# Optimization experiments

Measured on AMD Instinct MI355X. Metric: run time of the kernel, lower is better.

Reference implementation:

```python
import jax, jax.numpy as jnp
import numpy as np

MUL = 32      # multiplicity of each irrep type: 32x0e + 32x1o (dim = 32 + 96 = 128)
NSPEC = 10
NGRAPH = 16
EPS = 1e-5


def _split(x):
    # x: [N, 128] -> scalars [N, 32], vectors [N, 32, 3]
    return x[:, :MUL], x[:, MUL:].reshape(x.shape[0], MUL, 3)


def _cat(s, v):
    return jnp.concatenate([s, v.reshape(v.shape[0], MUL * 3)], axis=1)


def _irreps_linear(s, v, w0, w1, b0=None):
    # e3nn o3.Linear: per-irrep-type multiplicity mixing, /sqrt(fan_in), bias on scalars only
    inv = 1.0 / np.sqrt(MUL)
    s2 = s @ w0 * inv
    if b0 is not None:
        s2 = s2 + b0
    v2 = jnp.einsum('nuc,uw->nwc', v, w1) * inv
    return s2, v2


def _tensor_product(s1, v1, s2, v2, w000, w110, w011, w101):
    # SeparateWeightTensorProduct with per-path internal weights, lmax=1 paths:
    #   0e x 0e -> 0e, 1o x 1o -> 0e (CG = delta/sqrt(3)), 0e x 1o -> 1o, 1o x 0e -> 1o
    inv = 1.0 / np.sqrt(MUL * MUL)
    half = 1.0 / np.sqrt(2.0)  # two paths feed each output irrep
    out0 = (jnp.einsum('nu,nv,uvw->nw', s1, s2, w000)
            + jnp.einsum('nuc,nvc,uvw->nw', v1, v2, w110) / np.sqrt(3.0)) * (inv * half)
    out1 = (jnp.einsum('nu,nvc,uvw->nwc', s1, v2, w011)
            + jnp.einsum('nuc,nv,uvw->nwc', v1, s2, w101)) * (inv * half)
    return out0, out1


def _e3_layer_norm(s, v, batch, ln_w0, ln_b0, ln_w1):
    # per-graph equivariant layer norm: subtract mean on scalars, RMS-normalize each irrep field
    ones = jnp.ones(batch.shape, s.dtype)
    cnt = jnp.maximum(jax.ops.segment_sum(ones, batch, NGRAPH), 1.0)
    mean = jax.ops.segment_sum(s.sum(-1), batch, NGRAPH) / (cnt * MUL)
    s = s - mean[batch][:, None]
    n2s = jax.ops.segment_sum((s * s).sum(-1), batch, NGRAPH) / (cnt * MUL)
    s = s * jax.lax.rsqrt(n2s + EPS)[batch][:, None] * ln_w0 + ln_b0
    n2v = jax.ops.segment_sum((v * v).sum((-1, -2)), batch, NGRAPH) / (cnt * MUL)
    v = v * jax.lax.rsqrt(n2v + EPS)[batch][:, None, None] * ln_w1[None, :, None]
    return s, v


def setup_inputs() -> dict:
    key = jax.random.key(0)
    ks = jax.random.split(key, 24)
    N, B = 50000, 2
    rn = lambda k, sh: jax.random.normal(k, sh, dtype=jnp.float32)
    inp = {
        'node_feats_hidden': rn(ks[0], (B, N, MUL * 4)),
        'node_feats_up': rn(ks[1], (N, MUL * 4)),
        'hl_w0': rn(ks[2], (B, MUL, MUL)), 'hl_w1': rn(ks[3], (B, MUL, MUL)),
        'ul_w0': rn(ks[4], (B, MUL, MUL)), 'ul_w1': rn(ks[5], (B, MUL, MUL)),
        'tp_w000': rn(ks[6], (B, MUL, MUL, MUL)), 'tp_w110': rn(ks[7], (B, MUL, MUL, MUL)),
        'tp_w011': rn(ks[8], (B, MUL, MUL, MUL)), 'tp_w101': rn(ks[9], (B, MUL, MUL, MUL)),
        'lp_w0': rn(ks[10], (B, MUL, MUL)), 'lp_b0': jnp.zeros((B, MUL), jnp.float32),
        'lp_w1': rn(ks[11], (B, MUL, MUL)),
        'sc_w0': rn(ks[12], (B, MUL, NSPEC, MUL)), 'sc_w1': rn(ks[13], (B, MUL, NSPEC, MUL)),
        'ln_w0': jnp.ones((B, MUL), jnp.float32), 'ln_b0': jnp.zeros((B, MUL), jnp.float32),
        'ln_w1': jnp.ones((B, MUL), jnp.float32),
        'sk_w0': rn(ks[14], (B, MUL, MUL)), 'sk_b0': jnp.zeros((B, MUL), jnp.float32),
        'sk_w1': rn(ks[15], (B, MUL, MUL)),
        'node_species': jax.random.randint(ks[16], (N,), 0, NSPEC),
        'batch': jnp.sort(jax.random.randint(ks[17], (N,), 0, NGRAPH)),
    }
    return inp


def reference(node_feats_hidden, node_feats_up, hl_w0, hl_w1, ul_w0, ul_w1,
              tp_w000, tp_w110, tp_w011, tp_w101, lp_w0, lp_b0, lp_w1,
              sc_w0, sc_w1, ln_w0, ln_b0, ln_w1, sk_w0, sk_b0, sk_w1,
              node_species, batch):
    oh = jax.nn.one_hot(node_species, NSPEC, dtype=node_feats_up.dtype)
    inv_sc = 1.0 / np.sqrt(MUL * NSPEC)
    up = node_feats_up
    outs = []
    for b in range(node_feats_hidden.shape[0]):  # num_interactions blocks (fixed, small)
        sh, vh = _split(node_feats_hidden[b])
        su, vu = _split(up)
        shp, vhp = _irreps_linear(sh, vh, hl_w0[b], hl_w1[b])
        sup, vup = _irreps_linear(su, vu, ul_w0[b], ul_w1[b])
        z0, z1 = _tensor_product(shp, vhp, sup, vup,
                                 tp_w000[b], tp_w110[b], tp_w011[b], tp_w101[b])
        z0, z1 = _irreps_linear(z0, z1, lp_w0[b], lp_w1[b], lp_b0[b])
        # self connection: FullyConnectedTensorProduct(hidden, one-hot '10x0e', out)
        z0 = z0 + jnp.einsum('nu,nv,uvw->nw', sh, oh, sc_w0[b]) * inv_sc
        z1 = z1 + jnp.einsum('nuc,nv,uvw->nwc', vh, oh, sc_w1[b]) * inv_sc
        z0, z1 = _e3_layer_norm(z0, z1, batch, ln_w0[b], ln_b0[b], ln_w1[b])
        sk0, sk1 = _irreps_linear(sh, vh, sk_w0[b], sk_w1[b], sk_b0[b])
        out = _cat(z0 + sk0, z1 + sk1)
        outs.append(out)
        up = out  # next block consumes this block's output as node_feats_up
    return jnp.stack(outs)
```

## Files before the change

kernel.cpp:

```cpp
#include <hip/hip_runtime.h>
#include <math.h>

#define MULT 32
#define NSPEC 10
#define NGRAPH 16
#define NBANK 64
#define NCBANK 16
#define INV_SC 0.05590169943749474f
#define INV32S 0.17677669529663687f

typedef unsigned short u16;
typedef __bf16 v8bf __attribute__((ext_vector_type(8)));
typedef float v4f __attribute__((ext_vector_type(4)));
typedef unsigned int v4u_t __attribute__((ext_vector_type(4)));

__device__ __forceinline__ u16 f2bf(float f) {
    unsigned int u = __builtin_bit_cast(unsigned int, f);
    unsigned int r = u + 0x7fffu + ((u >> 16) & 1u);
    return (u16)(r >> 16);
}

__device__ __forceinline__ v8bf frag16(const u16* p) {
    return __builtin_bit_cast(v8bf, *(const v4u_t*)p);
}

#define MFMA(a, b, c) __builtin_amdgcn_mfma_f32_16x16x32_bf16(a, b, c, 0, 0, 0)

__global__ void zero_kernel(float* __restrict__ p, int n) {
    int i = blockIdx.x * 256 + threadIdx.x;
    if (i < n) p[i] = 0.0f;
}

__global__ void count_kernel(const int* __restrict__ batch, float* __restrict__ cntb, int N) {
    __shared__ int bins[NGRAPH];
    int t = threadIdx.x;
    if (t < NGRAPH) bins[t] = 0;
    __syncthreads();
    int i = blockIdx.x * 256 + t;
    if (i < N) atomicAdd(&bins[batch[i]], 1);
    __syncthreads();
    int bank = blockIdx.x & (NCBANK - 1);
    if (t < NGRAPH && bins[t] > 0) atomicAdd(&cntb[bank * NGRAPH + t], (float)bins[t]);
}

__global__ void stageA_kernel(const float* __restrict__ w000, const float* __restrict__ w110,
                              const float* __restrict__ w011, const float* __restrict__ w101,
                              const float* __restrict__ lp0, const float* __restrict__ lp1,
                              float* __restrict__ tmp1) {
    int gid = blockIdx.x * 256 + threadIdx.x;
    int tslot = gid >> 15;
    int e = gid & 32767;
    int z = e & 31;
    int uv = e >> 5;
    int b = tslot >> 2, path = tslot & 3;
    const float* W = (path == 0 ? w000 : path == 1 ? w110 : path == 2 ? w011 : w101) + b * 32768;
    const float* L = ((path == 0 || path == 1) ? lp0 : lp1) + b * 1024;
    float scale = (path == 1) ? (1.0f / (8192.0f * 1.7320508075688772f)) : (1.0f / 8192.0f);
    const float* wr = W + uv * 32;
    float acc = 0.0f;
    for (int w = 0; w < 32; ++w) acc += wr[w] * L[w * 32 + z];
    tmp1[gid] = acc * scale;
}

__global__ void stageB_kernel(const float* __restrict__ ul0, const float* __restrict__ ul1,
                              const float* __restrict__ tmp1, float* __restrict__ tmp2) {
    int gid = blockIdx.x * 256 + threadIdx.x;
    int tslot = gid >> 15;
    int e = gid & 32767;
    int z = e & 31;
    int bb = (e >> 5) & 31;
    int u = e >> 10;
    int b = tslot >> 2, path = tslot & 3;
    const float* U = ((path == 0 || path == 3) ? ul0 : ul1) + b * 1024;
    const float* in = tmp1 + (size_t)tslot * 32768 + u * 1024 + z;
    float acc = 0.0f;
    for (int v = 0; v < 32; ++v) acc += U[bb * 32 + v] * in[v * 32];
    tmp2[gid] = acc;
}

__global__ void stageC_kernel(const float* __restrict__ hl0, const float* __restrict__ hl1,
                              const float* __restrict__ tmp2, float* __restrict__ Weff) {
    int gid = blockIdx.x * 256 + threadIdx.x;
    int tslot = gid >> 15;
    int e = gid & 32767;
    int z = e & 31;
    int bb = (e >> 5) & 31;
    int a = e >> 10;
    int b = tslot >> 2, path = tslot & 3;
    const float* H = ((path == 0 || path == 2) ? hl0 : hl1) + b * 1024;
    const float* in = tmp2 + (size_t)tslot * 32768 + bb * 32 + z;
    float acc = 0.0f;
    for (int u = 0; u < 32; ++u) acc += H[a * 32 + u] * in[u * 1024];
    Weff[gid] = acc;
}

__global__ void pack_kernel(const float* __restrict__ Weff,
                            const float* __restrict__ sc_w0, const float* __restrict__ sc_w1,
                            u16* __restrict__ packs, int total) {
    int gid = blockIdx.x * 256 + threadIdx.x;
    if (gid >= total) return;
    int b = gid / 151552;
    int e = gid - b * 151552;
    float v;
    if (e < 131072) {
        int which = e >> 15;
        int e2 = e & 32767;
        int k = e2 & 31;
        int z = (e2 >> 5) & 31;
        int hi = e2 >> 10;
        int path = (which == 0) ? 0 : (which == 1) ? 2 : (which == 2) ? 3 : 1;
        int a  = (which < 2) ? k  : hi;
        int bb = (which < 2) ? hi : k;
        v = Weff[(size_t)((b * 4 + path) * 32 + a) * 1024 + bb * 32 + z];
    } else {
        int e2 = e - 131072;
        int which = e2 / 10240;
        int e3 = e2 - which * 10240;
        int s = e3 >> 10, z = (e3 >> 5) & 31, a = e3 & 31;
        const float* S = which ? sc_w1 : sc_w0;
        v = S[(size_t)b * 10240 + a * 320 + s * 32 + z] * INV_SC;
    }
    packs[gid] = f2bf(v);
}

__attribute__((amdgpu_waves_per_eu(4)))
__global__ __launch_bounds__(256)
void tp_kernel(const float* __restrict__ hidden_b, const float* __restrict__ up,
               const u16* __restrict__ pk,
               const float* __restrict__ lp_b0,
               const int* __restrict__ species, const int* __restrict__ batch,
               float* __restrict__ S1b, float* __restrict__ S2b, float* __restrict__ V2b,
               float* __restrict__ zout, int N) {
    constexpr int OFF_000 = 0, OFF_011 = 32768, OFF_101 = 65536, OFF_110 = 98304;
    constexpr int OFF_SC0 = 131072, OFF_SC1 = 141312;

    __shared__ __align__(16) char smem[24576];
    __shared__ int spec_l[16];
    __shared__ int bat_l[16];
    __shared__ float gs1[NGRAPH], gs2[NGRAPH], gv2[NGRAPH];

    u16* sh_bf = (u16*)smem;
    u16* su_bf = (u16*)(smem + 1280);
    u16* vu_bf = (u16*)(smem + 2560);
    u16* vh_bf = (u16*)(smem + 6400);
    float* suT = (float*)(smem + 10240);
    float* vuT = (float*)(smem + 12288);
    float* vhT = (float*)(smem + 18432);
    float* red = (float*)smem;

    const int t = threadIdx.x;
    const int w = t >> 6, lane = t & 63, quad = lane >> 4, c16 = lane & 15;
    const int n0 = blockIdx.x * 16;
    const int nvalid = min(16, N - n0);

    if (t < NGRAPH) { gs1[t] = 0.f; gs2[t] = 0.f; gv2[t] = 0.f; }
    if (t < 16) {
        spec_l[t] = (t < nvalid) ? species[n0 + t] : -1;
        bat_l[t]  = (t < nvalid) ? batch[n0 + t] : 0;
    }
    for (int i = t; i < 2048; i += 256) {
        int n = i >> 7, col = i & 127;
        float hv = 0.f, uv = 0.f;
        if (n < nvalid) {
            hv = hidden_b[(size_t)(n0 + n) * 128 + col];
            uv = up[(size_t)(n0 + n) * 128 + col];
        }
        if (col < 32) {
            sh_bf[n * 40 + col] = f2bf(hv); su_bf[n * 40 + col] = f2bf(uv);
            suT[col * 16 + n] = uv;
        } else {
            int idx = col - 32, c = idx % 3, a = idx / 3;
            vh_bf[(c * 16 + n) * 40 + a] = f2bf(hv);
            vu_bf[(c * 16 + n) * 40 + a] = f2bf(uv);
            vhT[(c * 32 + a) * 16 + n] = hv;
            vuT[(c * 32 + a) * 16 + n] = uv;
        }
    }
    __syncthreads();

    const v4f z4 = {0.f, 0.f, 0.f, 0.f};
    v4f o0[2];
    v4f o1[3][2];
    o0[0] = z4; o0[1] = z4;
#pragma unroll
    for (int c = 0; c < 3; ++c) { o1[c][0] = z4; o1[c][1] = z4; }

    v8bf a_sh = frag16(sh_bf + c16 * 40 + quad * 8);

    {
        const u16* Wb = pk + OFF_000 + (w * 16 * 16 + c16) * 32 + quad * 8;
#pragma unroll 4
        for (int th = 0; th < 8; ++th) {
            int bb = w * 8 + th;
            v4f y = *(const v4f*)(suT + bb * 16 + quad * 4);
            v8bf bf0 = frag16(Wb + (th * 2) * 512);
            v8bf bf1 = frag16(Wb + (th * 2 + 1) * 512);
            v4f C0 = MFMA(a_sh, bf0, z4);
            v4f C1 = MFMA(a_sh, bf1, z4);
#pragma unroll
            for (int r = 0; r < 4; ++r) {
                o0[0][r] += C0[r] * y[r];
                o0[1][r] += C1[r] * y[r];
            }
        }
    }
    {
        const u16* Wb = pk + OFF_011 + (w * 16 * 16 + c16) * 32 + quad * 8;
#pragma unroll 2
        for (int th = 0; th < 8; ++th) {
            int bb = w * 8 + th;
            v8bf bf0 = frag16(Wb + (th * 2) * 512);
            v8bf bf1 = frag16(Wb + (th * 2 + 1) * 512);
            v4f C0 = MFMA(a_sh, bf0, z4);
            v4f C1 = MFMA(a_sh, bf1, z4);
#pragma unroll
            for (int c = 0; c < 3; ++c) {
                v4f y = *(const v4f*)(vuT + (c * 32 + bb) * 16 + quad * 4);
#pragma unroll
                for (int r = 0; r < 4; ++r) {
                    o1[c][0][r] += C0[r] * y[r];
                    o1[c][1][r] += C1[r] * y[r];
                }
            }
        }
    }
    {
        v8bf a_su = frag16(su_bf + c16 * 40 + quad * 8);
        const u16* Wb = pk + OFF_101 + (w * 16 * 16 + c16) * 32 + quad * 8;
#pragma unroll 2
        for (int th = 0; th < 8; ++th) {
            int aa = w * 8 + th;
            v8bf bf0 = frag16(Wb + (th * 2) * 512);
            v8bf bf1 = frag16(Wb + (th * 2 + 1) * 512);
            v4f C0 = MFMA(a_su, bf0, z4);
            v4f C1 = MFMA(a_su, bf1, z4);
#pragma unroll
            for (int c = 0; c < 3; ++c) {
                v4f y = *(const v4f*)(vhT + (c * 32 + aa) * 16 + quad * 4);
#pragma unroll
                for (int r = 0; r < 4; ++r) {
                    o1[c][0][r] += C0[r] * y[r];
                    o1[c][1][r] += C1[r] * y[r];
                }
            }
        }
    }
    {
        v8bf av0 = frag16(vu_bf + (0 * 16 + c16) * 40 + quad * 8);
        v8bf av1 = frag16(vu_bf + (1 * 16 + c16) * 40 + quad * 8);
        v8bf av2 = frag16(vu_bf + (2 * 16 + c16) * 40 + quad * 8);
        const u16* Wb = pk + OFF_110 + (w * 16 * 16 + c16) * 32 + quad * 8;
#pragma unroll 2
        for (int th = 0; th < 8; ++th) {
            int aa = w * 8 + th;
            v8bf bf0 = frag16(Wb + (th * 2) * 512);
            v8bf bf1 = frag16(Wb + (th * 2 + 1) * 512);
            v4f y0 = *(const v4f*)(vhT + (0 * 32 + aa) * 16 + quad * 4);
            v4f y1 = *(const v4f*)(vhT + (1 * 32 + aa) * 16 + quad * 4);
            v4f y2 = *(const v4f*)(vhT + (2 * 32 + aa) * 16 + quad * 4);
            v4f C00 = MFMA(av0, bf0, z4), C01 = MFMA(av0, bf1, z4);
            v4f C10 = MFMA(av1, bf0, z4), C11 = MFMA(av1, bf1, z4);
            v4f C20 = MFMA(av2, bf0, z4), C21 = MFMA(av2, bf1, z4);
#pragma unroll
            for (int r = 0; r < 4; ++r) {
                o0[0][r] += C00[r] * y0[r] + C10[r] * y1[r] + C20[r] * y2[r];
                o0[1][r] += C01[r] * y0[r] + C11[r] * y1[r] + C21[r] * y2[r];
            }
        }
    }
    {
        const int s0 = (w < 2) ? w * 3 : 6 + (w - 2) * 2;
        const int ns = (w < 2) ? 3 : 2;
        v8bf zf = __builtin_bit_cast(v8bf, (v4u_t){0u, 0u, 0u, 0u});
        int sp = spec_l[c16];
        v8bf a_vh0 = frag16(vh_bf + (0 * 16 + c16) * 40 + quad * 8);
        v8bf a_vh1 = frag16(vh_bf + (1 * 16 + c16) * 40 + quad * 8);
        v8bf a_vh2 = frag16(vh_bf + (2 * 16 + c16) * 40 + quad * 8);
        for (int si = s0; si < s0 + ns; ++si) {
            bool m = (sp == si);
            v8bf ash_m = m ? a_sh : zf;
            v8bf am0 = m ? a_vh0 : zf;
            v8bf am1 = m ? a_vh1 : zf;
            v8bf am2 = m ? a_vh2 : zf;
#pragma unroll
            for (int zh = 0; zh < 2; ++zh) {
                int boff = (si * 32 + zh * 16 + c16) * 32 + quad * 8;
                v8bf bf0 = frag16(pk + OFF_SC0 + boff);
                v8bf bf1 = frag16(pk + OFF_SC1 + boff);
                o0[zh] = MFMA(ash_m, bf0, o0[zh]);
                o1[0][zh] = MFMA(am0, bf1, o1[0][zh]);
                o1[1][zh] = MFMA(am1, bf1, o1[1][zh]);
                o1[2][zh] = MFMA(am2, bf1, o1[2][zh]);
            }
        }
    }

    __syncthreads();
    if (w < 2) {
#pragma unroll
        for (int r = 0; r < 4; ++r) {
            int n = quad * 4 + r;
            float* row = red + (w * 16 + n) * 132;
            row[c16]      = o0[0][r];
            row[16 + c16] = o0[1][r];
#pragma unroll
            for (int c = 0; c < 3; ++c) {
                row[32 + c16 * 3 + c]        = o1[c][0][r];
                row[32 + (16 + c16) * 3 + c] = o1[c][1][r];
            }
        }
    }
    __syncthreads();
    if (w >= 2) {
#pragma unroll
        for (int r = 0; r < 4; ++r) {
            int n = quad * 4 + r;
            float* row = red + ((w - 2) * 16 + n) * 132;
            row[c16]      += o0[0][r];
            row[16 + c16] += o0[1][r];
#pragma unroll
            for (int c = 0; c < 3; ++c) {
                row[32 + c16 * 3 + c]        += o1[c][0][r];
                row[32 + (16 + c16) * 3 + c] += o1[c][1][r];
            }
        }
    }
    __syncthreads();
    {
        int n = t >> 4, seg = t & 15;
        v4f sa = z4, sb = z4;
#pragma unroll
        for (int ww = 0; ww < 2; ++ww) {
            const float* rp = red + (ww * 16 + n) * 132 + seg * 8;
            sa += *(const v4f*)rp;
            sb += *(const v4f*)(rp + 4);
        }
        float s1p = 0.f, s2p = 0.f, v2p = 0.f;
        if (seg < 4) {
            sa += *(const v4f*)(lp_b0 + seg * 8);
            sb += *(const v4f*)(lp_b0 + seg * 8 + 4);
            s1p = sa[0] + sa[1] + sa[2] + sa[3] + sb[0] + sb[1] + sb[2] + sb[3];
            s2p = sa[0]*sa[0] + sa[1]*sa[1] + sa[2]*sa[2] + sa[3]*sa[3]
                + sb[0]*sb[0] + sb[1]*sb[1] + sb[2]*sb[2] + sb[3]*sb[3];
        } else {
            v2p = sa[0]*sa[0] + sa[1]*sa[1] + sa[2]*sa[2] + sa[3]*sa[3]
                + sb[0]*sb[0] + sb[1]*sb[1] + sb[2]*sb[2] + sb[3]*sb[3];
        }
        if (n < nvalid) {
            float* op = zout + (size_t)(n0 + n) * 128 + seg * 8;
            *(v4f*)op = sa;
            *(v4f*)(op + 4) = sb;
        }
#pragma unroll
        for (int off = 8; off >= 1; off >>= 1) {
            s1p += __shfl_xor(s1p, off, 16);
            s2p += __shfl_xor(s2p, off, 16);
            v2p += __shfl_xor(v2p, off, 16);
        }
        if (seg == 0 && n < nvalid) {
            int g = bat_l[n];
            atomicAdd(&gs1[g], s1p);
            atomicAdd(&gs2[g], s2p);
            atomicAdd(&gv2[g], v2p);
        }
    }
    __syncthreads();
    {
        const int bank = blockIdx.x & (NBANK - 1);
        if (t < NGRAPH) {
            if (gs1[t] != 0.f) atomicAdd(&S1b[bank * NGRAPH + t], gs1[t]);
            if (gs2[t] != 0.f) atomicAdd(&S2b[bank * NGRAPH + t], gs2[t]);
            if (gv2[t] != 0.f) atomicAdd(&V2b[bank * NGRAPH + t], gv2[t]);
        }
    }
}

__global__ __launch_bounds__(256)
void norm_kernel(const float* __restrict__ hidden_b, float* __restrict__ out_b,
                 const float* __restrict__ skw0, const float* __restrict__ skb0,
                 const float* __restrict__ skw1,
                 const float* __restrict__ lnw0, const float* __restrict__ lnb0,
                 const float* __restrict__ lnw1,
                 const int* __restrict__ batch,
                 const float* __restrict__ S1b, const float* __restrict__ S2b,
                 const float* __restrict__ V2b, const float* __restrict__ cntb, int N) {
    __shared__ __align__(16) float sh_l[8][32];
    __shared__ __align__(16) float vh_l[8][96];
    __shared__ float stat_s[3][NGRAPH];
    __shared__ float cnt_s[NGRAPH];
    const int t = threadIdx.x, z = t & 31, nl = t >> 5;
    const int n0 = blockIdx.x * 8;
    for (int i = t; i < 8 * 128; i += 256) {
        int n = i >> 7, col = i & 127;
        float v = (n0 + n < N) ? hidden_b[(size_t)(n0 + n) * 128 + col] : 0.f;
        if (col < 32) sh_l[n][col] = v; else vh_l[n][col - 32] = v;
    }
    if (t < 48) {
        int arr = t >> 4, g = t & 15;
        const float* base = (arr == 0) ? S1b : (arr == 1) ? S2b : V2b;
        float s = 0.f;
        for (int k = 0; k < NBANK; ++k) s += base[k * NGRAPH + g];
        stat_s[arr][g] = s;
    } else if (t < 64) {
        int g = t - 48;
        float c = 0.f;
        for (int k = 0; k < NCBANK; ++k) c += cntb[k * NGRAPH + g];
        cnt_s[g] = c;
    }
    __syncthreads();
    const int n = n0 + nl;
    if (n >= N) return;

    float sk0 = 0.f, s1 = 0.f, s2 = 0.f, s3 = 0.f;
    for (int a = 0; a < 32; ++a) {
        float w0 = skw0[a * 32 + z];
        float w1 = skw1[a * 32 + z];
        sk0 += sh_l[nl][a] * w0;
        s1 += vh_l[nl][a * 3 + 0] * w1;
        s2 += vh_l[nl][a * 3 + 1] * w1;
        s3 += vh_l[nl][a * 3 + 2] * w1;
    }
    int g = batch[n];
    float cM = fmaxf(cnt_s[g], 1.0f) * 32.0f;
    float mean = stat_s[0][g] / cM;
    float var = fmaxf(stat_s[1][g] / cM - mean * mean, 0.0f);
    float rs = rsqrtf(var + 1e-5f);
    float rv = rsqrtf(fmaxf(stat_s[2][g] / cM, 0.0f) + 1e-5f);

    size_t base = (size_t)n * 128;
    float z0 = out_b[base + z];
    out_b[base + z] = (z0 - mean) * rs * lnw0[z] + lnb0[z] + sk0 * INV32S + skb0[z];
    float lw = lnw1[z] * rv;
    float x0 = out_b[base + 32 + z * 3 + 0];
    float x1 = out_b[base + 32 + z * 3 + 1];
    float x2 = out_b[base + 32 + z * 3 + 2];
    out_b[base + 32 + z * 3 + 0] = x0 * lw + s1 * INV32S;
    out_b[base + 32 + z * 3 + 1] = x1 * lw + s2 * INV32S;
    out_b[base + 32 + z * 3 + 2] = x2 * lw + s3 * INV32S;
}

extern "C" void kernel_launch(void* const* d_in, const int* in_sizes, int n_in,
                              void* d_out, int out_size, void* d_ws, size_t ws_size,
                              hipStream_t stream) {
    const float* hidden = (const float*)d_in[0];
    const float* up0    = (const float*)d_in[1];
    const float* hl_w0  = (const float*)d_in[2];
    const float* hl_w1  = (const float*)d_in[3];
    const float* ul_w0  = (const float*)d_in[4];
    const float* ul_w1  = (const float*)d_in[5];
    const float* w000   = (const float*)d_in[6];
    const float* w110   = (const float*)d_in[7];
    const float* w011   = (const float*)d_in[8];
    const float* w101   = (const float*)d_in[9];
    const float* lp_w0  = (const float*)d_in[10];
    const float* lp_b0  = (const float*)d_in[11];
    const float* lp_w1  = (const float*)d_in[12];
    const float* sc_w0  = (const float*)d_in[13];
    const float* sc_w1  = (const float*)d_in[14];
    const float* ln_w0  = (const float*)d_in[15];
    const float* ln_b0  = (const float*)d_in[16];
    const float* ln_w1  = (const float*)d_in[17];
    const float* sk_w0  = (const float*)d_in[18];
    const float* sk_b0  = (const float*)d_in[19];
    const float* sk_w1  = (const float*)d_in[20];
    const int* species  = (const int*)d_in[21];
    const int* batch    = (const int*)d_in[22];
    float* out = (float*)d_out;

    const int N = in_sizes[21];
    const int B = in_sizes[0] / (N * 128);

    float* ws = (float*)d_ws;
    float* tmp1 = ws;
    float* tmp2 = tmp1 + (size_t)B * 4 * 32768;
    float* cntb = tmp2 + (size_t)B * 4 * 32768;
    float* S1b = cntb + NCBANK * NGRAPH;
    float* S2b = S1b + (size_t)B * NBANK * NGRAPH;
    float* V2b = S2b + (size_t)B * NBANK * NGRAPH;
    int statn = NCBANK * NGRAPH + 3 * B * NBANK * NGRAPH;

    zero_kernel<<<(statn + 255) / 256, 256, 0, stream>>>(cntb, statn);
    count_kernel<<<(N + 255) / 256, 256, 0, stream>>>(batch, cntb, N);

    int nb = B * 4 * 32768 / 256;
    stageA_kernel<<<nb, 256, 0, stream>>>(w000, w110, w011, w101, lp_w0, lp_w1, tmp1);
    stageB_kernel<<<nb, 256, 0, stream>>>(ul_w0, ul_w1, tmp1, tmp2);
    stageC_kernel<<<nb, 256, 0, stream>>>(hl_w0, hl_w1, tmp2, tmp1);

    u16* packs = (u16*)tmp2;
    int ptotal = B * 151552;
    pack_kernel<<<(ptotal + 255) / 256, 256, 0, stream>>>(tmp1, sc_w0, sc_w1, packs, ptotal);

    for (int b = 0; b < B; ++b) {
        const float* up = (b == 0) ? up0 : out + (size_t)(b - 1) * N * 128;
        const u16* pb = packs + (size_t)b * 151552;
        tp_kernel<<<(N + 15) / 16, 256, 0, stream>>>(
            hidden + (size_t)b * N * 128, up, pb,
            lp_b0 + b * MULT, species, batch,
            S1b + (size_t)b * NBANK * NGRAPH, S2b + (size_t)b * NBANK * NGRAPH,
            V2b + (size_t)b * NBANK * NGRAPH,
            out + (size_t)b * N * 128, N);
        norm_kernel<<<(N + 7) / 8, 256, 0, stream>>>(
            hidden + (size_t)b * N * 128, out + (size_t)b * N * 128,
            sk_w0 + b * 1024, sk_b0 + b * MULT, sk_w1 + b * 1024,
            ln_w0 + b * MULT, ln_b0 + b * MULT, ln_w1 + b * MULT,
            batch, S1b + (size_t)b * NBANK * NGRAPH, S2b + (size_t)b * NBANK * NGRAPH,
            V2b + (size_t)b * NBANK * NGRAPH, cntb, N);
    }
}
```

Measured before the change: 385.2 us.

## Process two 16-node tiles per block to reuse weight fragments

```diff
diff --git a/kernel.cpp b/kernel.cpp
--- a/kernel.cpp
+++ b/kernel.cpp
@@ -123,7 +123,7 @@
     packs[gid] = f2bf(v);
 }
 
-__attribute__((amdgpu_waves_per_eu(4)))
+__attribute__((amdgpu_waves_per_eu(3)))
 __global__ __launch_bounds__(256)
 void tp_kernel(const float* __restrict__ hidden_b, const float* __restrict__ up,
                const u16* __restrict__ pk,
@@ -134,137 +134,164 @@
     constexpr int OFF_000 = 0, OFF_011 = 32768, OFF_101 = 65536, OFF_110 = 98304;
     constexpr int OFF_SC0 = 131072, OFF_SC1 = 141312;
 
-    __shared__ __align__(16) char smem[24576];
-    __shared__ int spec_l[16];
-    __shared__ int bat_l[16];
+    __shared__ __align__(16) char smem[49152];
+    __shared__ int spec_l[32];
+    __shared__ int bat_l[32];
     __shared__ float gs1[NGRAPH], gs2[NGRAPH], gv2[NGRAPH];
 
     u16* sh_bf = (u16*)smem;
-    u16* su_bf = (u16*)(smem + 1280);
-    u16* vu_bf = (u16*)(smem + 2560);
-    u16* vh_bf = (u16*)(smem + 6400);
-    float* suT = (float*)(smem + 10240);
-    float* vuT = (float*)(smem + 12288);
-    float* vhT = (float*)(smem + 18432);
+    u16* su_bf = (u16*)(smem + 2560);
+    u16* vu_bf = (u16*)(smem + 5120);
+    u16* vh_bf = (u16*)(smem + 12800);
+    float* suT = (float*)(smem + 20480);
+    float* vuT = (float*)(smem + 24576);
+    float* vhT = (float*)(smem + 36864);
     float* red = (float*)smem;
 
     const int t = threadIdx.x;
     const int w = t >> 6, lane = t & 63, quad = lane >> 4, c16 = lane & 15;
-    const int n0 = blockIdx.x * 16;
-    const int nvalid = min(16, N - n0);
+    const int n0 = blockIdx.x * 32;
+    const int nvalid = min(32, N - n0);
 
     if (t < NGRAPH) { gs1[t] = 0.f; gs2[t] = 0.f; gv2[t] = 0.f; }
-    if (t < 16) {
+    if (t < 32) {
         spec_l[t] = (t < nvalid) ? species[n0 + t] : -1;
         bat_l[t]  = (t < nvalid) ? batch[n0 + t] : 0;
     }
-    for (int i = t; i < 2048; i += 256) {
+    for (int i = t; i < 4096; i += 256) {
         int n = i >> 7, col = i & 127;
+        int tile = n >> 4, nl = n & 15;
         float hv = 0.f, uv = 0.f;
         if (n < nvalid) {
             hv = hidden_b[(size_t)(n0 + n) * 128 + col];
             uv = up[(size_t)(n0 + n) * 128 + col];
         }
         if (col < 32) {
-            sh_bf[n * 40 + col] = f2bf(hv); su_bf[n * 40 + col] = f2bf(uv);
-            suT[col * 16 + n] = uv;
+            sh_bf[tile * 640 + nl * 40 + col] = f2bf(hv);
+            su_bf[tile * 640 + nl * 40 + col] = f2bf(uv);
+            suT[tile * 512 + col * 16 + nl] = uv;
         } else {
             int idx = col - 32, c = idx % 3, a = idx / 3;
-            vh_bf[(c * 16 + n) * 40 + a] = f2bf(hv);
-            vu_bf[(c * 16 + n) * 40 + a] = f2bf(uv);
-            vhT[(c * 32 + a) * 16 + n] = hv;
-            vuT[(c * 32 + a) * 16 + n] = uv;
+            vh_bf[tile * 1920 + (c * 16 + nl) * 40 + a] = f2bf(hv);
+            vu_bf[tile * 1920 + (c * 16 + nl) * 40 + a] = f2bf(uv);
+            vhT[tile * 1536 + (c * 32 + a) * 16 + nl] = hv;
+            vuT[tile * 1536 + (c * 32 + a) * 16 + nl] = uv;
         }
     }
     __syncthreads();
 
     const v4f z4 = {0.f, 0.f, 0.f, 0.f};
-    v4f o0[2];
-    v4f o1[3][2];
-    o0[0] = z4; o0[1] = z4;
-#pragma unroll
-    for (int c = 0; c < 3; ++c) { o1[c][0] = z4; o1[c][1] = z4; }
-
-    v8bf a_sh = frag16(sh_bf + c16 * 40 + quad * 8);
-
-    {
-        const u16* Wb = pk + OFF_000 + (w * 16 * 16 + c16) * 32 + quad * 8;
+    v4f o0A[2], o1A[3][2], o0B[2], o1B[3][2];
+    o0A[0] = z4; o0A[1] = z4; o0B[0] = z4; o0B[1] = z4;
+#pragma unroll
+    for (int c = 0; c < 3; ++c) {
+        o1A[c][0] = z4; o1A[c][1] = z4;
+        o1B[c][0] = z4; o1B[c][1] = z4;
+    }
+
+    v8bf a_shA = frag16(sh_bf + c16 * 40 + quad * 8);
+    v8bf a_shB = frag16(sh_bf + 640 + c16 * 40 + quad * 8);
+
+    {
+        const u16* Wb = pk + OFF_000 + (w * 256 + c16) * 32 + quad * 8;
 #pragma unroll 4
         for (int th = 0; th < 8; ++th) {
             int bb = w * 8 + th;
-            v4f y = *(const v4f*)(suT + bb * 16 + quad * 4);
             v8bf bf0 = frag16(Wb + (th * 2) * 512);
             v8bf bf1 = frag16(Wb + (th * 2 + 1) * 512);
-            v4f C0 = MFMA(a_sh, bf0, z4);
-            v4f C1 = MFMA(a_sh, bf1, z4);
+            v4f yA = *(const v4f*)(suT + bb * 16 + quad * 4);
+            v4f yB = *(const v4f*)(suT + 512 + bb * 16 + quad * 4);
+            v4f C0 = MFMA(a_shA, bf0, z4), C1 = MFMA(a_shA, bf1, z4);
+            v4f D0 = MFMA(a_shB, bf0, z4), D1 = MFMA(a_shB, bf1, z4);
 #pragma unroll
             for (int r = 0; r < 4; ++r) {
-                o0[0][r] += C0[r] * y[r];
-                o0[1][r] += C1[r] * y[r];
-            }
-        }
-    }
-    {
-        const u16* Wb = pk + OFF_011 + (w * 16 * 16 + c16) * 32 + quad * 8;
+                o0A[0][r] += C0[r] * yA[r]; o0A[1][r] += C1[r] * yA[r];
+                o0B[0][r] += D0[r] * yB[r]; o0B[1][r] += D1[r] * yB[r];
+            }
+        }
+    }
+    {
+        const u16* Wb = pk + OFF_011 + (w * 256 + c16) * 32 + quad * 8;
 #pragma unroll 2
         for (int th = 0; th < 8; ++th) {
             int bb = w * 8 + th;
             v8bf bf0 = frag16(Wb + (th * 2) * 512);
             v8bf bf1 = frag16(Wb + (th * 2 + 1) * 512);
-            v4f C0 = MFMA(a_sh, bf0, z4);
-            v4f C1 = MFMA(a_sh, bf1, z4);
+            v4f C0 = MFMA(a_shA, bf0, z4), C1 = MFMA(a_shA, bf1, z4);
+            v4f D0 = MFMA(a_shB, bf0, z4), D1 = MFMA(a_shB, bf1, z4);
 #pragma unroll
             for (int c = 0; c < 3; ++c) {
-                v4f y = *(const v4f*)(vuT + (c * 32 + bb) * 16 + quad * 4);
+                v4f yA = *(const v4f*)(vuT + (c * 32 + bb) * 16 + quad * 4);
+                v4f yB = *(const v4f*)(vuT + 1536 + (c * 32 + bb) * 16 + quad * 4);
 #pragma unroll
                 for (int r = 0; r < 4; ++r) {
-                    o1[c][0][r] += C0[r] * y[r];
-                    o1[c][1][r] += C1[r] * y[r];
+                    o1A[c][0][r] += C0[r] * yA[r]; o1A[c][1][r] += C1[r] * yA[r];
+                    o1B[c][0][r] += D0[r] * yB[r]; o1B[c][1][r] += D1[r] * yB[r];
                 }
             }
         }
     }
     {
-        v8bf a_su = frag16(su_bf + c16 * 40 + quad * 8);
-        const u16* Wb = pk + OFF_101 + (w * 16 * 16 + c16) * 32 + quad * 8;
+        v8bf a_suA = frag16(su_bf + c16 * 40 + quad * 8);
+        v8bf a_suB = frag16(su_bf + 640 + c16 * 40 + quad * 8);
+        const u16* Wb = pk + OFF_101 + (w * 256 + c16) * 32 + quad * 8;
 #pragma unroll 2
         for (int th = 0; th < 8; ++th) {
             int aa = w * 8 + th;
             v8bf bf0 = frag16(Wb + (th * 2) * 512);
             v8bf bf1 = frag16(Wb + (th * 2 + 1) * 512);
-            v4f C0 = MFMA(a_su, bf0, z4);
-            v4f C1 = MFMA(a_su, bf1, z4);
+            v4f C0 = MFMA(a_suA, bf0, z4), C1 = MFMA(a_suA, bf1, z4);
+            v4f D0 = MFMA(a_suB, bf0, z4), D1 = MFMA(a_suB, bf1, z4);
 #pragma unroll
             for (int c = 0; c < 3; ++c) {
-                v4f y = *(const v4f*)(vhT + (c * 32 + aa) * 16 + quad * 4);
+                v4f yA = *(const v4f*)(vhT + (c * 32 + aa) * 16 + quad * 4);
+                v4f yB = *(const v4f*)(vhT + 1536 + (c * 32 + aa) * 16 + quad * 4);
 #pragma unroll
                 for (int r = 0; r < 4; ++r) {
-                    o1[c][0][r] += C0[r] * y[r];
-                    o1[c][1][r] += C1[r] * y[r];
+                    o1A[c][0][r] += C0[r] * yA[r]; o1A[c][1][r] += C1[r] * yA[r];
+                    o1B[c][0][r] += D0[r] * yB[r]; o1B[c][1][r] += D1[r] * yB[r];
                 }
             }
         }
     }
     {
-        v8bf av0 = frag16(vu_bf + (0 * 16 + c16) * 40 + quad * 8);
-        v8bf av1 = frag16(vu_bf + (1 * 16 + c16) * 40 + quad * 8);
-        v8bf av2 = frag16(vu_bf + (2 * 16 + c16) * 40 + quad * 8);
-        const u16* Wb = pk + OFF_110 + (w * 16 * 16 + c16) * 32 + quad * 8;
+        v8bf avA0 = frag16(vu_bf + (0 * 16 + c16) * 40 + quad * 8);
+        v8bf avA1 = frag16(vu_bf + (1 * 16 + c16) * 40 + quad * 8);
+        v8bf avA2 = frag16(vu_bf + (2 * 16 + c16) * 40 + quad * 8);
+        v8bf avB0 = frag16(vu_bf + 1920 + (0 * 16 + c16) * 40 + quad * 8);
+        v8bf avB1 = frag16(vu_bf + 1920 + (1 * 16 + c16) * 40 + quad * 8);
+        v8bf avB2 = frag16(vu_bf + 1920 + (2 * 16 + c16) * 40 + quad * 8);
+        const u16* Wb = pk + OFF_110 + (w * 256 + c16) * 32 + quad * 8;
 #pragma unroll 2
         for (int th = 0; th < 8; ++th) {
             int aa = w * 8 + th;
             v8bf bf0 = frag16(Wb + (th * 2) * 512);
             v8bf bf1 = frag16(Wb + (th * 2 + 1) * 512);
-            v4f y0 = *(const v4f*)(vhT + (0 * 32 + aa) * 16 + quad * 4);
-            v4f y1 = *(const v4f*)(vhT + (1 * 32 + aa) * 16 + quad * 4);
-            v4f y2 = *(const v4f*)(vhT + (2 * 32 + aa) * 16 + quad * 4);
-            v4f C00 = MFMA(av0, bf0, z4), C01 = MFMA(av0, bf1, z4);
-            v4f C10 = MFMA(av1, bf0, z4), C11 = MFMA(av1, bf1, z4);
-            v4f C20 = MFMA(av2, bf0, z4), C21 = MFMA(av2, bf1, z4);
-#pragma unroll
-            for (int r = 0; r < 4; ++r) {
-                o0[0][r] += C00[r] * y0[r] + C10[r] * y1[r] + C20[r] * y2[r];
-                o0[1][r] += C01[r] * y0[r] + C11[r] * y1[r] + C21[r] * y2[r];
+            {
+                v4f y0 = *(const v4f*)(vhT + (0 * 32 + aa) * 16 + quad * 4);
+                v4f y1 = *(const v4f*)(vhT + (1 * 32 + aa) * 16 + quad * 4);
+                v4f y2 = *(const v4f*)(vhT + (2 * 32 + aa) * 16 + quad * 4);
+                v4f C00 = MFMA(avA0, bf0, z4), C01 = MFMA(avA0, bf1, z4);
+                v4f C10 = MFMA(avA1, bf0, z4), C11 = MFMA(avA1, bf1, z4);
+                v4f C20 = MFMA(avA2, bf0, z4), C21 = MFMA(avA2, bf1, z4);
+#pragma unroll
+                for (int r = 0; r < 4; ++r) {
+                    o0A[0][r] += C00[r] * y0[r] + C10[r] * y1[r] + C20[r] * y2[r];
+                    o0A[1][r] += C01[r] * y0[r] + C11[r] * y1[r] + C21[r] * y2[r];
+                }
+            }
+            {
+                v4f y0 = *(const v4f*)(vhT + 1536 + (0 * 32 + aa) * 16 + quad * 4);
+                v4f y1 = *(const v4f*)(vhT + 1536 + (1 * 32 + aa) * 16 + quad * 4);
+                v4f y2 = *(const v4f*)(vhT + 1536 + (2 * 32 + aa) * 16 + quad * 4);
+                v4f C00 = MFMA(avB0, bf0, z4), C01 = MFMA(avB0, bf1, z4);
+                v4f C10 = MFMA(avB1, bf0, z4), C11 = MFMA(avB1, bf1, z4);
+                v4f C20 = MFMA(avB2, bf0, z4), C21 = MFMA(avB2, bf1, z4);
+#pragma unroll
+                for (int r = 0; r < 4; ++r) {
+                    o0B[0][r] += C00[r] * y0[r] + C10[r] * y1[r] + C20[r] * y2[r];
+                    o0B[1][r] += C01[r] * y0[r] + C11[r] * y1[r] + C21[r] * y2[r];
+                }
             }
         }
     }
@@ -272,25 +299,37 @@
         const int s0 = (w < 2) ? w * 3 : 6 + (w - 2) * 2;
         const int ns = (w < 2) ? 3 : 2;
         v8bf zf = __builtin_bit_cast(v8bf, (v4u_t){0u, 0u, 0u, 0u});
-        int sp = spec_l[c16];
-        v8bf a_vh0 = frag16(vh_bf + (0 * 16 + c16) * 40 + quad * 8);
-        v8bf a_vh1 = frag16(vh_bf + (1 * 16 + c16) * 40 + quad * 8);
-        v8bf a_vh2 = frag16(vh_bf + (2 * 16 + c16) * 40 + quad * 8);
+        int spA = spec_l[c16];
+        int spB = spec_l[16 + c16];
+        v8bf a_vhA0 = frag16(vh_bf + (0 * 16 + c16) * 40 + quad * 8);
+        v8bf a_vhA1 = frag16(vh_bf + (1 * 16 + c16) * 40 + quad * 8);
+        v8bf a_vhA2 = frag16(vh_bf + (2 * 16 + c16) * 40 + quad * 8);
+        v8bf a_vhB0 = frag16(vh_bf + 1920 + (0 * 16 + c16) * 40 + quad * 8);
+        v8bf a_vhB1 = frag16(vh_bf + 1920 + (1 * 16 + c16) * 40 + quad * 8);
+        v8bf a_vhB2 = frag16(vh_bf + 1920 + (2 * 16 + c16) * 40 + quad * 8);
         for (int si = s0; si < s0 + ns; ++si) {
-            bool m = (sp == si);
-            v8bf ash_m = m ? a_sh : zf;
-            v8bf am0 = m ? a_vh0 : zf;
-            v8bf am1 = m ? a_vh1 : zf;
-            v8bf am2 = m ? a_vh2 : zf;
+            bool mA = (spA == si), mB = (spB == si);
+            v8bf ashA_m = mA ? a_shA : zf;
+            v8bf amA0 = mA ? a_vhA0 : zf;
+            v8bf amA1 = mA ? a_vhA1 : zf;
+            v8bf amA2 = mA ? a_vhA2 : zf;
+            v8bf ashB_m = mB ? a_shB : zf;
+            v8bf amB0 = mB ? a_vhB0 : zf;
+            v8bf amB1 = mB ? a_vhB1 : zf;
+            v8bf amB2 = mB ? a_vhB2 : zf;
 #pragma unroll
             for (int zh = 0; zh < 2; ++zh) {
                 int boff = (si * 32 + zh * 16 + c16) * 32 + quad * 8;
                 v8bf bf0 = frag16(pk + OFF_SC0 + boff);
                 v8bf bf1 = frag16(pk + OFF_SC1 + boff);
-                o0[zh] = MFMA(ash_m, bf0, o0[zh]);
-                o1[0][zh] = MFMA(am0, bf1, o1[0][zh]);
-                o1[1][zh] = MFMA(am1, bf1, o1[1][zh]);
-                o1[2][zh] = MFMA(am2, bf1, o1[2][zh]);
+                o0A[zh] = MFMA(ashA_m, bf0, o0A[zh]);
+                o1A[0][zh] = MFMA(amA0, bf1, o1A[0][zh]);
+                o1A[1][zh] = MFMA(amA1, bf1, o1A[1][zh]);
+                o1A[2][zh] = MFMA(amA2, bf1, o1A[2][zh]);
+                o0B[zh] = MFMA(ashB_m, bf0, o0B[zh]);
+                o1B[0][zh] = MFMA(amB0, bf1, o1B[0][zh]);
+                o1B[1][zh] = MFMA(amB1, bf1, o1B[1][zh]);
+                o1B[2][zh] = MFMA(amB2, bf1, o1B[2][zh]);
             }
         }
     }
@@ -300,13 +339,18 @@
 #pragma unroll
         for (int r = 0; r < 4; ++r) {
             int n = quad * 4 + r;
-            float* row = red + (w * 16 + n) * 132;
-            row[c16]      = o0[0][r];
-            row[16 + c16] = o0[1][r];
+            float* rowA = red + (w * 32 + n) * 132;
+            float* rowB = red + (w * 32 + 16 + n) * 132;
+            rowA[c16]      = o0A[0][r];
+            rowA[16 + c16] = o0A[1][r];
+            rowB[c16]      = o0B[0][r];
+            rowB[16 + c16] = o0B[1][r];
 #pragma unroll
             for (int c = 0; c < 3; ++c) {
-                row[32 + c16 * 3 + c]        = o1[c][0][r];
-                row[32 + (16 + c16) * 3 + c] = o1[c][1][r];
+                rowA[32 + c16 * 3 + c]        = o1A[c][0][r];
+                rowA[32 + (16 + c16) * 3 + c] = o1A[c][1][r];
+                rowB[32 + c16 * 3 + c]        = o1B[c][0][r];
+                rowB[32 + (16 + c16) * 3 + c] = o1B[c][1][r];
             }
         }
     }
@@ -315,53 +359,62 @@
 #pragma unroll
         for (int r = 0; r < 4; ++r) {
             int n = quad * 4 + r;
-            float* row = red + ((w - 2) * 16 + n) * 132;
-            row[c16]      += o0[0][r];
-            row[16 + c16] += o0[1][r];
+            float* rowA = red + ((w - 2) * 32 + n) * 132;
+            float* rowB = red + ((w - 2) * 32 + 16 + n) * 132;
+            rowA[c16]      += o0A[0][r];
+            rowA[16 + c16] += o0A[1][r];
+            rowB[c16]      += o0B[0][r];
+            rowB[16 + c16] += o0B[1][r];
 #pragma unroll
             for (int c = 0; c < 3; ++c) {
-                row[32 + c16 * 3 + c]        += o1[c][0][r];
-                row[32 + (16 + c16) * 3 + c] += o1[c][1][r];
-            }
-        }
-    }
-    __syncthreads();
-    {
-        int n = t >> 4, seg = t & 15;
-        v4f sa = z4, sb = z4;
-#pragma unroll
-        for (int ww = 0; ww < 2; ++ww) {
-            const float* rp = red + (ww * 16 + n) * 132 + seg * 8;
-            sa += *(const v4f*)rp;
-            sb += *(const v4f*)(rp + 4);
-        }
-        float s1p = 0.f, s2p = 0.f, v2p = 0.f;
-        if (seg < 4) {
-            sa += *(const v4f*)(lp_b0 + seg * 8);
-            sb += *(const v4f*)(lp_b0 + seg * 8 + 4);
-            s1p = sa[0] + sa[1] + sa[2] + sa[3] + sb[0] + sb[1] + sb[2] + sb[3];
-            s2p = sa[0]*sa[0] + sa[1]*sa[1] + sa[2]*sa[2] + sa[3]*sa[3]
-                + sb[0]*sb[0] + sb[1]*sb[1] + sb[2]*sb[2] + sb[3]*sb[3];
-        } else {
-            v2p = sa[0]*sa[0] + sa[1]*sa[1] + sa[2]*sa[2] + sa[3]*sa[3]
-                + sb[0]*sb[0] + sb[1]*sb[1] + sb[2]*sb[2] + sb[3]*sb[3];
-        }
-        if (n < nvalid) {
-            float* op = zout + (size_t)(n0 + n) * 128 + seg * 8;
-            *(v4f*)op = sa;
-            *(v4f*)(op + 4) = sb;
-        }
-#pragma unroll
-        for (int off = 8; off >= 1; off >>= 1) {
-            s1p += __shfl_xor(s1p, off, 16);
-            s2p += __shfl_xor(s2p, off, 16);
-            v2p += __shfl_xor(v2p, off, 16);
-        }
-        if (seg == 0 && n < nvalid) {
-            int g = bat_l[n];
-            atomicAdd(&gs1[g], s1p);
-            atomicAdd(&gs2[g], s2p);
-            atomicAdd(&gv2[g], v2p);
+                rowA[32 + c16 * 3 + c]        += o1A[c][0][r];
+                rowA[32 + (16 + c16) * 3 + c] += o1A[c][1][r];
+                rowB[32 + c16 * 3 + c]        += o1B[c][0][r];
+                rowB[32 + (16 + c16) * 3 + c] += o1B[c][1][r];
+            }
+        }
+    }
+    __syncthreads();
+    {
+        int nl = t >> 4, seg = t & 15;
+#pragma unroll
+        for (int tile = 0; tile < 2; ++tile) {
+            int node = tile * 16 + nl;
+            v4f sa = z4, sb = z4;
+#pragma unroll
+            for (int ww = 0; ww < 2; ++ww) {
+                const float* rp = red + (ww * 32 + node) * 132 + seg * 8;
+                sa += *(const v4f*)rp;
+                sb += *(const v4f*)(rp + 4);
+            }
+            float s1p = 0.f, s2p = 0.f, v2p = 0.f;
+            if (seg < 4) {
+                sa += *(const v4f*)(lp_b0 + seg * 8);
+                sb += *(const v4f*)(lp_b0 + seg * 8 + 4);
+                s1p = sa[0] + sa[1] + sa[2] + sa[3] + sb[0] + sb[1] + sb[2] + sb[3];
+                s2p = sa[0]*sa[0] + sa[1]*sa[1] + sa[2]*sa[2] + sa[3]*sa[3]
+                    + sb[0]*sb[0] + sb[1]*sb[1] + sb[2]*sb[2] + sb[3]*sb[3];
+            } else {
+                v2p = sa[0]*sa[0] + sa[1]*sa[1] + sa[2]*sa[2] + sa[3]*sa[3]
+                    + sb[0]*sb[0] + sb[1]*sb[1] + sb[2]*sb[2] + sb[3]*sb[3];
+            }
+            if (node < nvalid) {
+                float* op = zout + (size_t)(n0 + node) * 128 + seg * 8;
+                *(v4f*)op = sa;
+                *(v4f*)(op + 4) = sb;
+            }
+#pragma unroll
+            for (int off = 8; off >= 1; off >>= 1) {
+                s1p += __shfl_xor(s1p, off, 16);
+                s2p += __shfl_xor(s2p, off, 16);
+                v2p += __shfl_xor(v2p, off, 16);
+            }
+            if (seg == 0 && node < nvalid) {
+                int g = bat_l[node];
+                atomicAdd(&gs1[g], s1p);
+                atomicAdd(&gs2[g], s2p);
+                atomicAdd(&gv2[g], v2p);
+            }
         }
     }
     __syncthreads();
@@ -494,7 +547,7 @@
     for (int b = 0; b < B; ++b) {
         const float* up = (b == 0) ? up0 : out + (size_t)(b - 1) * N * 128;
         const u16* pb = packs + (size_t)b * 151552;
-        tp_kernel<<<(N + 15) / 16, 256, 0, stream>>>(
+        tp_kernel<<<(N + 31) / 32, 256, 0, stream>>>(
             hidden + (size_t)b * N * 128, up, pb,
             lp_b0 + b * MULT, species, batch,
             S1b + (size_t)b * NBANK * NGRAPH, S2b + (size_t)b * NBANK * NGRAPH,
```

New measurement: 381.4 us. About the same (-1.0%).

## Stream TP weight fragments through per-wave LDS ring via async global_load_lds

Applied to the files above, without the earlier changes.

```diff
diff --git a/kernel.cpp b/kernel.cpp
--- a/kernel.cpp
+++ b/kernel.cpp
@@ -25,6 +25,10 @@
 }
 
 #define MFMA(a, b, c) __builtin_amdgcn_mfma_f32_16x16x32_bf16(a, b, c, 0, 0, 0)
+
+#define GLL(g, l) __builtin_amdgcn_global_load_lds( \
+    (const __attribute__((address_space(1))) unsigned int*)(g), \
+    (__attribute__((address_space(3))) unsigned int*)(l), 16, 0, 0)
 
 __global__ void zero_kernel(float* __restrict__ p, int n) {
     int i = blockIdx.x * 256 + threadIdx.x;
@@ -131,10 +135,9 @@
                const int* __restrict__ species, const int* __restrict__ batch,
                float* __restrict__ S1b, float* __restrict__ S2b, float* __restrict__ V2b,
                float* __restrict__ zout, int N) {
-    constexpr int OFF_000 = 0, OFF_011 = 32768, OFF_101 = 65536, OFF_110 = 98304;
     constexpr int OFF_SC0 = 131072, OFF_SC1 = 141312;
 
-    __shared__ __align__(16) char smem[24576];
+    __shared__ __align__(16) char smem[57344];
     __shared__ int spec_l[16];
     __shared__ int bat_l[16];
     __shared__ float gs1[NGRAPH], gs2[NGRAPH], gv2[NGRAPH];
@@ -147,11 +150,24 @@
     float* vuT = (float*)(smem + 12288);
     float* vhT = (float*)(smem + 18432);
     float* red = (float*)smem;
+    u16* wring = (u16*)(smem + 24576);
 
     const int t = threadIdx.x;
     const int w = t >> 6, lane = t & 63, quad = lane >> 4, c16 = lane & 15;
     const int n0 = blockIdx.x * 16;
     const int nvalid = min(16, N - n0);
+
+    const u16* pkw = pk + (w * 256 + c16) * 32 + quad * 8;
+    u16* myring = wring + w * 4096;
+
+#define ISSUE(g) do { \
+        const u16* gsrc_ = pkw + ((g) >> 3) * 32768 + ((g) & 7) * 1024; \
+        u16* l_ = myring + (((g) & 3) << 10); \
+        GLL(gsrc_, l_); \
+        GLL(gsrc_ + 512, l_ + 512); \
+    } while (0)
+
+    ISSUE(0); ISSUE(1); ISSUE(2);
 
     if (t < NGRAPH) { gs1[t] = 0.f; gs2[t] = 0.f; gv2[t] = 0.f; }
     if (t < 16) {
@@ -187,87 +203,113 @@
 
     v8bf a_sh = frag16(sh_bf + c16 * 40 + quad * 8);
 
+#pragma unroll 1
+    for (int s = 0; s < 8; ++s) {
+        asm volatile("s_waitcnt vmcnt(4)" ::: "memory");
+        const u16* rp = myring + ((s & 3) << 10);
+        v8bf wf0 = frag16(rp + lane * 8);
+        v8bf wf1 = frag16(rp + 512 + lane * 8);
+        const int hi = w * 8 + s;
+        v4f y = *(const v4f*)(suT + hi * 16 + quad * 4);
+        v4f C0 = MFMA(a_sh, wf0, z4);
+        v4f C1 = MFMA(a_sh, wf1, z4);
+#pragma unroll
+        for (int r = 0; r < 4; ++r) {
+            o0[0][r] += C0[r] * y[r];
+            o0[1][r] += C1[r] * y[r];
+        }
+        ISSUE(s + 3);
+    }
+#pragma unroll 1
+    for (int s = 0; s < 8; ++s) {
+        asm volatile("s_waitcnt vmcnt(4)" ::: "memory");
+        const u16* rp = myring + ((s & 3) << 10);
+        v8bf wf0 = frag16(rp + lane * 8);
+        v8bf wf1 = frag16(rp + 512 + lane * 8);
+        const int hi = w * 8 + s;
+        v4f C0 = MFMA(a_sh, wf0, z4);
+        v4f C1 = MFMA(a_sh, wf1, z4);
+#pragma unroll
+        for (int c = 0; c < 3; ++c) {
+            v4f y = *(const v4f*)(vuT + (c * 32 + hi) * 16 + quad * 4);
+#pragma unroll
+            for (int r = 0; r < 4; ++r) {
+                o1[c][0][r] += C0[r] * y[r];
+                o1[c][1][r] += C1[r] * y[r];
+            }
+        }
+        ISSUE(s + 11);
+    }
     {
-        const u16* Wb = pk + OFF_000 + (w * 16 * 16 + c16) * 32 + quad * 8;
-#pragma unroll 4
-        for (int th = 0; th < 8; ++th) {
-            int bb = w * 8 + th;
-            v4f y = *(const v4f*)(suT + bb * 16 + quad * 4);
-            v8bf bf0 = frag16(Wb + (th * 2) * 512);
-            v8bf bf1 = frag16(Wb + (th * 2 + 1) * 512);
-            v4f C0 = MFMA(a_sh, bf0, z4);
-            v4f C1 = MFMA(a_sh, bf1, z4);
-#pragma unroll
-            for (int r = 0; r < 4; ++r) {
-                o0[0][r] += C0[r] * y[r];
-                o0[1][r] += C1[r] * y[r];
-            }
-        }
-    }
-    {
-        const u16* Wb = pk + OFF_011 + (w * 16 * 16 + c16) * 32 + quad * 8;
-#pragma unroll 2
-        for (int th = 0; th < 8; ++th) {
-            int bb = w * 8 + th;
-            v8bf bf0 = frag16(Wb + (th * 2) * 512);
-            v8bf bf1 = frag16(Wb + (th * 2 + 1) * 512);
-            v4f C0 = MFMA(a_sh, bf0, z4);
-            v4f C1 = MFMA(a_sh, bf1, z4);
+        v8bf a_su = frag16(su_bf + c16 * 40 + quad * 8);
+#pragma unroll 1
+        for (int s = 0; s < 8; ++s) {
+            asm volatile("s_waitcnt vmcnt(4)" ::: "memory");
+            const u16* rp = myring + ((s & 3) << 10);
+            v8bf wf0 = frag16(rp + lane * 8);
+            v8bf wf1 = frag16(rp + 512 + lane * 8);
+            const int hi = w * 8 + s;
+            v4f C0 = MFMA(a_su, wf0, z4);
+            v4f C1 = MFMA(a_su, wf1, z4);
 #pragma unroll
             for (int c = 0; c < 3; ++c) {
-                v4f y = *(const v4f*)(vuT + (c * 32 + bb) * 16 + quad * 4);
+                v4f y = *(const v4f*)(vhT + (c * 32 + hi) * 16 + quad * 4);
 #pragma unroll
                 for (int r = 0; r < 4; ++r) {
                     o1[c][0][r] += C0[r] * y[r];
                     o1[c][1][r] += C1[r] * y[r];
                 }
             }
-        }
-    }
-    {
-        v8bf a_su = frag16(su_bf + c16 * 40 + quad * 8);
-        const u16* Wb = pk + OFF_101 + (w * 16 * 16 + c16) * 32 + quad * 8;
-#pragma unroll 2
-        for (int th = 0; th < 8; ++th) {
-            int aa = w * 8 + th;
-            v8bf bf0 = frag16(Wb + (th * 2) * 512);
-            v8bf bf1 = frag16(Wb + (th * 2 + 1) * 512);
-            v4f C0 = MFMA(a_su, bf0, z4);
-            v4f C1 = MFMA(a_su, bf1, z4);
-#pragma unroll
-            for (int c = 0; c < 3; ++c) {
-                v4f y = *(const v4f*)(vhT + (c * 32 + aa) * 16 + quad * 4);
-#pragma unroll
-                for (int r = 0; r < 4; ++r) {
-                    o1[c][0][r] += C0[r] * y[r];
-                    o1[c][1][r] += C1[r] * y[r];
-                }
-            }
+            ISSUE(s + 19);
         }
     }
     {
         v8bf av0 = frag16(vu_bf + (0 * 16 + c16) * 40 + quad * 8);
         v8bf av1 = frag16(vu_bf + (1 * 16 + c16) * 40 + quad * 8);
         v8bf av2 = frag16(vu_bf + (2 * 16 + c16) * 40 + quad * 8);
-        const u16* Wb = pk + OFF_110 + (w * 16 * 16 + c16) * 32 + quad * 8;
-#pragma unroll 2
-        for (int th = 0; th < 8; ++th) {
-            int aa = w * 8 + th;
-            v8bf bf0 = frag16(Wb + (th * 2) * 512);
-            v8bf bf1 = frag16(Wb + (th * 2 + 1) * 512);
-            v4f y0 = *(const v4f*)(vhT + (0 * 32 + aa) * 16 + quad * 4);
-            v4f y1 = *(const v4f*)(vhT + (1 * 32 + aa) * 16 + quad * 4);
-            v4f y2 = *(const v4f*)(vhT + (2 * 32 + aa) * 16 + quad * 4);
-            v4f C00 = MFMA(av0, bf0, z4), C01 = MFMA(av0, bf1, z4);
-            v4f C10 = MFMA(av1, bf0, z4), C11 = MFMA(av1, bf1, z4);
-            v4f C20 = MFMA(av2, bf0, z4), C21 = MFMA(av2, bf1, z4);
+#pragma unroll 1
+        for (int s = 0; s < 6; ++s) {
+            asm volatile("s_waitcnt vmcnt(4)" ::: "memory");
+            const u16* rp = myring + ((s & 3) << 10);
+            v8bf wf0 = frag16(rp + lane * 8);
+            v8bf wf1 = frag16(rp + 512 + lane * 8);
+            const int hi = w * 8 + s;
+            v4f y0 = *(const v4f*)(vhT + (0 * 32 + hi) * 16 + quad * 4);
+            v4f y1 = *(const v4f*)(vhT + (1 * 32 + hi) * 16 + quad * 4);
+            v4f y2 = *(const v4f*)(vhT + (2 * 32 + hi) * 16 + quad * 4);
+            v4f C00 = MFMA(av0, wf0, z4), C01 = MFMA(av0, wf1, z4);
+            v4f C10 = MFMA(av1, wf0, z4), C11 = MFMA(av1, wf1, z4);
+            v4f C20 = MFMA(av2, wf0, z4), C21 = MFMA(av2, wf1, z4);
 #pragma unroll
             for (int r = 0; r < 4; ++r) {
                 o0[0][r] += C00[r] * y0[r] + C10[r] * y1[r] + C20[r] * y2[r];
                 o0[1][r] += C01[r] * y0[r] + C11[r] * y1[r] + C21[r] * y2[r];
             }
-        }
-    }
+            if (s < 5) ISSUE(s + 27);
+        }
+#pragma unroll
+        for (int s = 6; s < 8; ++s) {
+            if (s == 6) { asm volatile("s_waitcnt vmcnt(2)" ::: "memory"); }
+            else       { asm volatile("s_waitcnt vmcnt(0)" ::: "memory"); }
+            const u16* rp = myring + ((s & 3) << 10);
+            v8bf wf0 = frag16(rp + lane * 8);
+            v8bf wf1 = frag16(rp + 512 + lane * 8);
+            const int hi = w * 8 + s;
+            v4f y0 = *(const v4f*)(vhT + (0 * 32 + hi) * 16 + quad * 4);
+            v4f y1 = *(const v4f*)(vhT + (1 * 32 + hi) * 16 + quad * 4);
+            v4f y2 = *(const v4f*)(vhT + (2 * 32 + hi) * 16 + quad * 4);
+            v4f C00 = MFMA(av0, wf0, z4), C01 = MFMA(av0, wf1, z4);
+            v4f C10 = MFMA(av1, wf0, z4), C11 = MFMA(av1, wf1, z4);
+            v4f C20 = MFMA(av2, wf0, z4), C21 = MFMA(av2, wf1, z4);
+#pragma unroll
+            for (int r = 0; r < 4; ++r) {
+                o0[0][r] += C00[r] * y0[r] + C10[r] * y1[r] + C20[r] * y2[r];
+                o0[1][r] += C01[r] * y0[r] + C11[r] * y1[r] + C21[r] * y2[r];
+            }
+        }
+    }
+#undef ISSUE
+
     {
         const int s0 = (w < 2) ? w * 3 : 6 + (w - 2) * 2;
         const int ns = (w < 2) ? 3 : 2;
```

After: 434.5 us. 1.13x slower.
